# Kernel optimization log

Measured on AMD Instinct MI355X. Metric: run time of the kernel, lower is better.

Reference implementation:

```python
import jax, jax.numpy as jnp
import numpy as np

V, H, HALF, L, B = 32000, 512, 256, 1024, 64
LN_EPS = 1e-5
DELTA_EPS = 1e-6


def _forward(seq, embed, ff_w1, ff_b1, ff_w2, ff_b2, ln_g, ln_b,
             sem_w, sem_b, epi_w, epi_b, out_w, out_b):
    # Encoder: embed -> residual FFN -> LayerNorm
    e = embed[seq]                                   # (B, L, H)
    ff = jax.nn.relu(e @ ff_w1 + ff_b1) @ ff_w2 + ff_b2
    x = e + ff
    mu = jnp.mean(x, axis=-1, keepdims=True)
    var = jnp.mean((x - mu) ** 2, axis=-1, keepdims=True)
    h = (x - mu) / jnp.sqrt(var + LN_EPS) * ln_g + ln_b  # (B, L, H)

    # Project all timesteps at once (batched GEMM instead of per-step Linear)
    ks_all = h @ sem_w + sem_b                       # (B, L, half)
    ke_all = h @ epi_w + epi_b                       # (B, L, half)

    Bsz = seq.shape[0]
    Ls = seq.shape[1]
    w_t = jnp.arange(1, Ls, dtype=h.dtype) / Ls      # (L-1,) linear recency weights

    def step(carry, inp):
        M_s, M_e = carry
        k_s, k_e, w = inp                            # (B, half), (B, half), scalar
        vps = jnp.einsum('bij,bj->bi', M_s, k_s)
        dvs = k_s - vps / (jnp.sum(k_s * k_s, axis=-1, keepdims=True) + DELTA_EPS)
        M_s = M_s + dvs[:, :, None] * k_s[:, None, :]
        vpe = jnp.einsum('bij,bj->bi', M_e, k_e)
        dve = k_e - vpe / (jnp.sum(k_e * k_e, axis=-1, keepdims=True) + DELTA_EPS)
        M_e = M_e + w * (dve[:, :, None] * k_e[:, None, :])
        return (M_s, M_e), None

    M0 = jnp.zeros((Bsz, HALF, HALF), dtype=h.dtype)
    xs = (jnp.swapaxes(ks_all[:, :-1], 0, 1),        # (L-1, B, half)
          jnp.swapaxes(ke_all[:, :-1], 0, 1),
          w_t)
    (M_s, M_e), _ = jax.lax.scan(step, (M0, M0), xs)

    cs = jnp.einsum('bij,bj->bi', M_s, ks_all[:, -1])
    ce = jnp.einsum('bij,bj->bi', M_e, ke_all[:, -1])
    return jnp.concatenate([cs, ce], axis=-1) @ out_w + out_b  # (B, V)


def setup_inputs() -> dict:
    key = jax.random.key(0)
    ks = jax.random.split(key, 8)
    n = lambda k, shape, s=0.02: jax.random.normal(k, shape, jnp.float32) * s
    return {
        'seq': jax.random.randint(ks[0], (B, L), 0, V),
        'embed': n(ks[1], (V, H)),
        'ff_w1': n(ks[2], (H, 2 * H)), 'ff_b1': jnp.zeros((2 * H,), jnp.float32),
        'ff_w2': n(ks[3], (2 * H, H)), 'ff_b2': jnp.zeros((H,), jnp.float32),
        'ln_g': jnp.ones((H,), jnp.float32), 'ln_b': jnp.zeros((H,), jnp.float32),
        'sem_w': n(ks[4], (H, HALF)), 'sem_b': jnp.zeros((HALF,), jnp.float32),
        'epi_w': n(ks[5], (H, HALF)), 'epi_b': jnp.zeros((HALF,), jnp.float32),
        'out_w': n(ks[6], (2 * HALF, V)), 'out_b': jnp.zeros((V,), jnp.float32),
    }


def reference(seq, embed, ff_w1, ff_b1, ff_w2, ff_b2, ln_g, ln_b,
              sem_w, sem_b, epi_w, epi_b, out_w, out_b):
    return _forward(seq, embed, ff_w1, ff_b1, ff_w2, ff_b2, ln_g, ln_b,
                    sem_w, sem_b, epi_w, epi_b, out_w, out_b)
```

## Files before the change

### kernel.cpp

```cpp
#include <hip/hip_runtime.h>

typedef unsigned short ushort_t;
typedef unsigned int uint_t;
typedef __attribute__((ext_vector_type(8))) short short8;
typedef __attribute__((ext_vector_type(4))) float f32x4;

static constexpr int V = 32000, H = 512, HALFD = 256, LSEQ = 1024, BB = 64;

__device__ __forceinline__ ushort_t f2bf(float f) {
    uint_t u = __float_as_uint(f);
    u = (u + 0x7FFFu + ((u >> 16) & 1u)) >> 16;
    return (ushort_t)u;
}
__device__ __forceinline__ float bf2f(ushort_t u) {
    return __uint_as_float(((uint_t)u) << 16);
}
__device__ __forceinline__ float bflo(uint_t u) { return __uint_as_float(u << 16); }
__device__ __forceinline__ float bfhi(uint_t u) { return __uint_as_float(u & 0xffff0000u); }
__device__ __forceinline__ float bfres(float v) { return v - bf2f(f2bf(v)); }

typedef const __attribute__((address_space(1))) void* gas_ptr;
typedef __attribute__((address_space(3))) void* las_ptr;
#define GLDS16(g, l) __builtin_amdgcn_global_load_lds((gas_ptr)(g), (las_ptr)(l), 16, 0, 0)

__device__ __forceinline__ const short8* rd64(const ushort_t* b, int row, int chunk) {
    return (const short8*)(b + row * 32 + (((chunk ^ ((row >> 1) & 3)) & 3) << 3));
}
__device__ __forceinline__ ushort_t* wr64(ushort_t* b, int row, int chunk) {
    return b + row * 32 + (((chunk ^ ((row >> 1) & 3)) & 3) << 3);
}

__global__ void transpose_cvt(const float* __restrict__ W, ushort_t* __restrict__ Wt,
                              int K, int N) {
    __shared__ float tile[32][33];
    int k0 = blockIdx.y * 32, n0 = blockIdx.x * 32;
    int tx = threadIdx.x & 31, ty = threadIdx.x >> 5;
    #pragma unroll
    for (int i = 0; i < 32; i += 8)
        tile[ty + i][tx] = W[(size_t)(k0 + ty + i) * N + n0 + tx];
    __syncthreads();
    #pragma unroll
    for (int i = 0; i < 32; i += 8)
        Wt[(size_t)(n0 + ty + i) * K + k0 + tx] = f2bf(tile[tx][ty + i]);
}

__global__ __launch_bounds__(256) void gemm_ffn1(
        const int* __restrict__ seqp, const float* __restrict__ embed,
        const ushort_t* __restrict__ Bt, const float* __restrict__ bias,
        ushort_t* __restrict__ Cout, int N, int K) {
    __shared__ __align__(16) ushort_t Al[2048];
    __shared__ __align__(16) ushort_t Bl[4096];
    int t = threadIdx.x;
    int m0 = blockIdx.y * 64, n0 = blockIdx.x * 128;
    int lane = t & 63, wid = t >> 6;
    int wm = (wid & 1) * 32, wn = (wid >> 1) * 64;
    int lid = lane & 15, quad = lane >> 4;
    int srow = t >> 2;
    int gch = (t & 3) ^ ((t >> 3) & 3);

    int tok0 = seqp[m0 + srow];
    const float* e0 = embed + (size_t)tok0 * H + (t & 3) * 8;
    const ushort_t* b0p = Bt + (size_t)(n0 + srow) * K + gch * 8;
    const ushort_t* b1p = Bt + (size_t)(n0 + 64 + srow) * K + gch * 8;
    ushort_t* ldsB = Bl + wid * 512;
    ushort_t* aw0 = wr64(Al, srow, t & 3);

    f32x4 acc[2][4];
    #pragma unroll
    for (int i = 0; i < 2; ++i)
        #pragma unroll
        for (int j = 0; j < 4; ++j)
            acc[i][j] = (f32x4){0.f, 0.f, 0.f, 0.f};

    for (int k0 = 0; k0 < K; k0 += 32) {
        __syncthreads();
        GLDS16(b0p + k0, ldsB);
        GLDS16(b1p + k0, ldsB + 2048);
        float4 ea0 = *(const float4*)(e0 + k0);
        float4 eb0 = *(const float4*)(e0 + k0 + 4);
        short8 s0;
        s0[0] = (short)f2bf(ea0.x); s0[1] = (short)f2bf(ea0.y);
        s0[2] = (short)f2bf(ea0.z); s0[3] = (short)f2bf(ea0.w);
        s0[4] = (short)f2bf(eb0.x); s0[5] = (short)f2bf(eb0.y);
        s0[6] = (short)f2bf(eb0.z); s0[7] = (short)f2bf(eb0.w);
        *(short8*)aw0 = s0;
        __syncthreads();
        short8 af[2], bfr[4];
        #pragma unroll
        for (int i = 0; i < 2; ++i) af[i] = *rd64(Al, wm + i * 16 + lid, quad);
        #pragma unroll
        for (int i = 0; i < 4; ++i) bfr[i] = *rd64(Bl, wn + i * 16 + lid, quad);
        #pragma unroll
        for (int mt = 0; mt < 2; ++mt)
            #pragma unroll
            for (int nt = 0; nt < 4; ++nt)
                acc[mt][nt] = __builtin_amdgcn_mfma_f32_16x16x32_bf16(
                    af[mt], bfr[nt], acc[mt][nt], 0, 0, 0);
    }
    #pragma unroll
    for (int mt = 0; mt < 2; ++mt)
        #pragma unroll
        for (int nt = 0; nt < 4; ++nt)
            #pragma unroll
            for (int rg = 0; rg < 4; ++rg) {
                int row = m0 + wm + mt * 16 + quad * 4 + rg;
                int col = n0 + wn + nt * 16 + lid;
                float v = fmaxf(acc[mt][nt][rg] + bias[col], 0.f);
                Cout[(size_t)row * N + col] = f2bf(v);
            }
}

__global__ __launch_bounds__(256) void gemm_ffn2(
        const ushort_t* __restrict__ A, const ushort_t* __restrict__ Bt,
        const float* __restrict__ bias, const int* __restrict__ seqp,
        const float* __restrict__ embed, ushort_t* __restrict__ Cout,
        int N, int K) {
    __shared__ __align__(16) ushort_t Al[2048];
    __shared__ __align__(16) ushort_t Bl[4096];
    int t = threadIdx.x;
    int m0 = blockIdx.y * 64, n0 = blockIdx.x * 128;
    int lane = t & 63, wid = t >> 6;
    int wm = (wid & 1) * 32, wn = (wid >> 1) * 64;
    int lid = lane & 15, quad = lane >> 4;
    int srow = t >> 2;
    int gch = (t & 3) ^ ((t >> 3) & 3);

    const ushort_t* a0p = A + (size_t)(m0 + srow) * K + gch * 8;
    const ushort_t* b0p = Bt + (size_t)(n0 + srow) * K + gch * 8;
    const ushort_t* b1p = Bt + (size_t)(n0 + 64 + srow) * K + gch * 8;
    ushort_t* ldsA = Al + wid * 512;
    ushort_t* ldsB = Bl + wid * 512;

    f32x4 acc[2][4];
    #pragma unroll
    for (int i = 0; i < 2; ++i)
        #pragma unroll
        for (int j = 0; j < 4; ++j)
            acc[i][j] = (f32x4){0.f, 0.f, 0.f, 0.f};

    for (int k0 = 0; k0 < K; k0 += 32) {
        __syncthreads();
        GLDS16(a0p + k0, ldsA);
        GLDS16(b0p + k0, ldsB);
        GLDS16(b1p + k0, ldsB + 2048);
        __syncthreads();
        short8 af[2], bfr[4];
        #pragma unroll
        for (int i = 0; i < 2; ++i) af[i] = *rd64(Al, wm + i * 16 + lid, quad);
        #pragma unroll
        for (int i = 0; i < 4; ++i) bfr[i] = *rd64(Bl, wn + i * 16 + lid, quad);
        #pragma unroll
        for (int mt = 0; mt < 2; ++mt)
            #pragma unroll
            for (int nt = 0; nt < 4; ++nt)
                acc[mt][nt] = __builtin_amdgcn_mfma_f32_16x16x32_bf16(
                    af[mt], bfr[nt], acc[mt][nt], 0, 0, 0);
    }
    #pragma unroll
    for (int mt = 0; mt < 2; ++mt)
        #pragma unroll
        for (int rg = 0; rg < 4; ++rg) {
            int row = m0 + wm + mt * 16 + quad * 4 + rg;
            int tok = seqp[row];
            const float* erow = embed + (size_t)tok * H;
            #pragma unroll
            for (int nt = 0; nt < 4; ++nt) {
                int col = n0 + wn + nt * 16 + lid;
                float v = acc[mt][nt][rg] + bias[col] + erow[col];
                Cout[(size_t)row * N + col] = f2bf(v);
            }
        }
}

__global__ __launch_bounds__(256) void gemm_proj(
        const ushort_t* __restrict__ A, const ushort_t* __restrict__ Bt,
        const float* __restrict__ biasS, const float* __restrict__ biasE,
        ushort_t* __restrict__ outS, ushort_t* __restrict__ outE, int K) {
    __shared__ __align__(16) ushort_t Al[2048];
    __shared__ __align__(16) ushort_t Bl[4096];
    int t = threadIdx.x;
    int m0 = blockIdx.y * 64, n0 = blockIdx.x * 128;
    int lane = t & 63, wid = t >> 6;
    int wm = (wid & 1) * 32, wn = (wid >> 1) * 64;
    int lid = lane & 15, quad = lane >> 4;
    int srow = t >> 2;
    int gch = (t & 3) ^ ((t >> 3) & 3);

    const ushort_t* a0p = A + (size_t)(m0 + srow) * K + gch * 8;
    const ushort_t* b0p = Bt + (size_t)(n0 + srow) * K + gch * 8;
    const ushort_t* b1p = Bt + (size_t)(n0 + 64 + srow) * K + gch * 8;
    ushort_t* ldsA = Al + wid * 512;
    ushort_t* ldsB = Bl + wid * 512;

    f32x4 acc[2][4];
    #pragma unroll
    for (int i = 0; i < 2; ++i)
        #pragma unroll
        for (int j = 0; j < 4; ++j)
            acc[i][j] = (f32x4){0.f, 0.f, 0.f, 0.f};

    for (int k0 = 0; k0 < K; k0 += 32) {
        __syncthreads();
        GLDS16(a0p + k0, ldsA);
        GLDS16(b0p + k0, ldsB);
        GLDS16(b1p + k0, ldsB + 2048);
        __syncthreads();
        short8 af[2], bfr[4];
        #pragma unroll
        for (int i = 0; i < 2; ++i) af[i] = *rd64(Al, wm + i * 16 + lid, quad);
        #pragma unroll
        for (int i = 0; i < 4; ++i) bfr[i] = *rd64(Bl, wn + i * 16 + lid, quad);
        #pragma unroll
        for (int mt = 0; mt < 2; ++mt)
            #pragma unroll
            for (int nt = 0; nt < 4; ++nt)
                acc[mt][nt] = __builtin_amdgcn_mfma_f32_16x16x32_bf16(
                    af[mt], bfr[nt], acc[mt][nt], 0, 0, 0);
    }
    #pragma unroll
    for (int mt = 0; mt < 2; ++mt)
        #pragma unroll
        for (int nt = 0; nt < 4; ++nt)
            #pragma unroll
            for (int rg = 0; rg < 4; ++rg) {
                int row = m0 + wm + mt * 16 + quad * 4 + rg;
                int col = n0 + wn + nt * 16 + lid;
                if (col < 256)
                    outS[(size_t)row * HALFD + col] = f2bf(acc[mt][nt][rg] + biasS[col]);
                else
                    outE[(size_t)row * HALFD + col - 256] =
                        f2bf(acc[mt][nt][rg] + biasE[col - 256]);
            }
}

__global__ void ln_kernel(ushort_t* X, const float* __restrict__ g,
                          const float* __restrict__ bta) {
    int row = blockIdx.x * 4 + (threadIdx.x >> 6);
    int lane = threadIdx.x & 63;
    ushort_t* xr = X + (size_t)row * H + lane * 8;
    short8 xv = *(short8*)xr;
    float x[8];
    #pragma unroll
    for (int j = 0; j < 8; ++j) x[j] = bf2f((ushort_t)xv[j]);
    float s = 0.f, ss = 0.f;
    #pragma unroll
    for (int j = 0; j < 8; ++j) { s += x[j]; ss += x[j] * x[j]; }
    #pragma unroll
    for (int d = 1; d < 64; d <<= 1) { s += __shfl_xor(s, d); ss += __shfl_xor(ss, d); }
    float mu = s * (1.f / 512.f);
    float var = ss * (1.f / 512.f) - mu * mu;
    float rstd = rsqrtf(var + 1e-5f);
    float4 g0 = *(const float4*)(g + lane * 8);
    float4 g1 = *(const float4*)(g + lane * 8 + 4);
    float4 b0 = *(const float4*)(bta + lane * 8);
    float4 b1 = *(const float4*)(bta + lane * 8 + 4);
    float gg[8] = {g0.x, g0.y, g0.z, g0.w, g1.x, g1.y, g1.z, g1.w};
    float bb[8] = {b0.x, b0.y, b0.z, b0.w, b1.x, b1.y, b1.z, b1.w};
    short8 o;
    #pragma unroll
    for (int j = 0; j < 8; ++j)
        o[j] = (short)f2bf((x[j] - mu) * rstd * gg[j] + bb[j]);
    *(short8*)xr = o;
}

__global__ void beta_kernel(const ushort_t* __restrict__ k, float* __restrict__ beta) {
    int row = blockIdx.x * 4 + (threadIdx.x >> 6);
    int lane = threadIdx.x & 63;
    ushort4 a = *(const ushort4*)(k + (size_t)row * HALFD + lane * 4);
    float ax = bf2f(a.x), ay = bf2f(a.y), az = bf2f(a.z), aw = bf2f(a.w);
    float s = ax * ax + ay * ay + az * az + aw * aw;
    #pragma unroll
    for (int d = 1; d < 64; d <<= 1) s += __shfl_xor(s, d);
    if (lane == 0) beta[row] = s + 1e-6f;
}

__global__ __launch_bounds__(256) void tinv_kernel(
        const ushort_t* __restrict__ ks, const ushort_t* __restrict__ ke,
        const float* __restrict__ beta_s, const float* __restrict__ beta_e,
        ushort_t* __restrict__ Dg) {
    __shared__ __align__(16) ushort_t Kl[64][280];
    __shared__ __align__(16) ushort_t LmT[4][64][66];
    __shared__ float betsl[4][64];

    int t = threadIdx.x;
    int lane = t & 63, wv = t >> 6;
    int lid = lane & 15, quad = lane >> 4;
    int blk0 = blockIdx.x * 4;
    const float invL = 1.0f / 1024.0f;

    for (int pp = 0; pp < 4; ++pp) {
        int p = blk0 + pp;
        int ch = p & 15, bm = p >> 4;
        int mat = bm & 1, b = bm >> 1;
        const ushort_t* Kp = (mat ? ke : ks) + ((size_t)b * LSEQ + ch * 64) * HALFD;
        const float* Bp = (mat ? beta_e : beta_s) + (size_t)b * LSEQ + ch * 64;

        __syncthreads();
        {
            int j = t >> 2, c0 = (t & 3) * 64;
            const ushort_t* src = Kp + (size_t)j * HALFD + c0;
            #pragma unroll
            for (int x = 0; x < 8; ++x)
                *(short8*)&Kl[j][c0 + x * 8] = *(const short8*)(src + x * 8);
        }
        if (t < 64) betsl[pp][t] = Bp[t];
        __syncthreads();

        f32x4 g[4];
        #pragma unroll
        for (int i = 0; i < 4; ++i) g[i] = (f32x4){0.f, 0.f, 0.f, 0.f};
        #pragma unroll
        for (int kc = 0; kc < 8; ++kc) {
            short8 af = *(const short8*)&Kl[wv * 16 + lid][kc * 32 + quad * 8];
            #pragma unroll
            for (int nt = 0; nt < 4; ++nt) {
                short8 bq = *(const short8*)&Kl[nt * 16 + lid][kc * 32 + quad * 8];
                g[nt] = __builtin_amdgcn_mfma_f32_16x16x32_bf16(af, bq, g[nt], 0, 0, 0);
            }
        }
        #pragma unroll
        for (int nt = 0; nt < 4; ++nt)
            #pragma unroll
            for (int rg = 0; rg < 4; ++rg) {
                int i = wv * 16 + quad * 4 + rg;
                int j = nt * 16 + lid;
                int s = ch * 64 + i;
                float wgt = mat ? (float)(s + 1) * invL : 1.0f;
                if (s >= 1023) wgt = 0.f;
                float wb = wgt / betsl[pp][i];
                LmT[pp][j][i] = f2bf((j < i) ? g[nt][rg] * wb : 0.f);
            }
    }
    __syncthreads();

    const ushort_t (*Lp)[66] = LmT[wv];
    float a[64];
    #pragma unroll
    for (int x = 0; x < 32; ++x) {
        uint_t u = *(const uint_t*)&Lp[lane][x * 2];
        a[x * 2]     = -bflo(u);
        a[x * 2 + 1] = -bfhi(u);
    }
    #pragma unroll
    for (int j = 0; j < 63; ++j) {
        float dj = a[j];
        const ushort_t* rowj = Lp[j];
        #pragma unroll
        for (int ii = (j + 1) & ~1; ii < 64; ii += 2) {
            uint_t u = *(const uint_t*)&rowj[ii];
            if (ii > j) a[ii] -= bflo(u) * dj;
            a[ii + 1]        -= bfhi(u) * dj;
        }
    }
    size_t pbase = (size_t)(blk0 + wv) * 4096;
    #pragma unroll
    for (int i = 0; i < 64; ++i)
// ... 192 lines not shown
    }

    __syncthreads();
    float* vsc = (float*)RHSl;
    float kvv[4];
    #pragma unroll
    for (int nt = 0; nt < 4; ++nt)
        kvv[nt] = bf2f(Kl[63][wn + nt * 16 + lid]);
    #pragma unroll
    for (int mt = 0; mt < 4; ++mt)
        #pragma unroll
        for (int rg = 0; rg < 4; ++rg) {
            float p = acc[mt][0][rg] * kvv[0] + acc[mt][1][rg] * kvv[1]
                    + acc[mt][2][rg] * kvv[2] + acc[mt][3][rg] * kvv[3];
            p += __shfl_xor(p, 1); p += __shfl_xor(p, 2);
            p += __shfl_xor(p, 4); p += __shfl_xor(p, 8);
            if (lid == 0)
                vsc[(wid >> 1) * 128 + wm + mt * 16 + quad * 4 + rg] = p;
        }
    __syncthreads();
    if (t < 128) {
        float sum = vsc[t] + vsc[128 + t] + vsc[256 + t] + vsc[384 + t];
        c[(size_t)b * 512 + mat * 256 + half * 128 + t] = sum;
    }
}

__global__ __launch_bounds__(512) void out_gemm(
        const float* __restrict__ c, const float* __restrict__ W,
        const float* __restrict__ bias, float* __restrict__ out) {
    __shared__ __align__(16) float cl[16][512];
    int t = threadIdx.x;
    int lane = t & 63, w = t >> 6;
    int cb = blockIdx.x * 256;
    int rb = blockIdx.y * 16;

    #pragma unroll
    for (int i = 0; i < 4; ++i) {
        int idx = t + i * 512;
        int row = idx >> 7, c4 = (idx & 127) * 4;
        *(float4*)&cl[row][c4] = *(const float4*)(c + (size_t)(rb + row) * 512 + c4);
    }
    __syncthreads();

    const float* wp = W + cb + lane * 4;
    int r0 = w * 2;
    f32x4 a0 = (f32x4){0.f, 0.f, 0.f, 0.f};
    f32x4 a1 = (f32x4){0.f, 0.f, 0.f, 0.f};

    #pragma unroll 2
    for (int k = 0; k < 512; k += 4) {
        f32x4 w0 = *(const f32x4*)(wp + (size_t)(k + 0) * V);
        f32x4 w1 = *(const f32x4*)(wp + (size_t)(k + 1) * V);
        f32x4 w2 = *(const f32x4*)(wp + (size_t)(k + 2) * V);
        f32x4 w3 = *(const f32x4*)(wp + (size_t)(k + 3) * V);
        f32x4 ca = *(const f32x4*)&cl[r0][k];
        f32x4 cb4 = *(const f32x4*)&cl[r0 + 1][k];
        a0 += ca[0] * w0; a0 += ca[1] * w1; a0 += ca[2] * w2; a0 += ca[3] * w3;
        a1 += cb4[0] * w0; a1 += cb4[1] * w1; a1 += cb4[2] * w2; a1 += cb4[3] * w3;
    }
    f32x4 bv = *(const f32x4*)(bias + cb + lane * 4);
    *(f32x4*)(out + (size_t)(rb + r0) * V + cb + lane * 4) = a0 + bv;
    *(f32x4*)(out + (size_t)(rb + r0 + 1) * V + cb + lane * 4) = a1 + bv;
}

extern "C" void kernel_launch(void* const* d_in, const int* in_sizes, int n_in,
                              void* d_out, int out_size, void* d_ws, size_t ws_size,
                              hipStream_t stream) {
    const int*   seq    = (const int*)d_in[0];
    const float* embed  = (const float*)d_in[1];
    const float* ff_w1  = (const float*)d_in[2];
    const float* ff_b1  = (const float*)d_in[3];
    const float* ff_w2  = (const float*)d_in[4];
    const float* ff_b2  = (const float*)d_in[5];
    const float* ln_g   = (const float*)d_in[6];
    const float* ln_b   = (const float*)d_in[7];
    const float* sem_w  = (const float*)d_in[8];
    const float* sem_b  = (const float*)d_in[9];
    const float* epi_w  = (const float*)d_in[10];
    const float* epi_b  = (const float*)d_in[11];
    const float* out_w  = (const float*)d_in[12];
    const float* out_b  = (const float*)d_in[13];
    float* outp = (float*)d_out;

    const int ML = BB * LSEQ;
    int RCH;
    if      (ws_size >= 271712256ull) RCH = 65536;
    else if (ws_size >= 120717312ull) RCH = 16384;
    else                              RCH = 8192;

    char* w = (char*)d_ws;
    size_t off = 0;
    ushort_t* ks_bf = (ushort_t*)(w + off); off += 33554432;
    ushort_t* ke_bf = (ushort_t*)(w + off); off += 33554432;
    ushort_t* ebc   = (ushort_t*)(w + off); off += (size_t)RCH * 512 * 2;
    ushort_t* t1c   = (ushort_t*)(w + off); off += (size_t)RCH * 1024 * 2;
    ushort_t* w1t   = (ushort_t*)(w + off); off += 1048576;
    ushort_t* w2t   = (ushort_t*)(w + off); off += 1048576;
    ushort_t* semt  = (ushort_t*)(w + off); off += 262144;
    ushort_t* epit  = (ushort_t*)(w + off); off += 262144;
    float*    bet_s = (float*)(w + off);    off += 262144;
    float*    bet_e = (float*)(w + off);    off += 262144;
    float*    cbuf  = (float*)(w + off);    off += 131072;
    ushort_t* Dbuf  = ebc;
    (void)t1c;

    transpose_cvt<<<dim3(1024 / 32, 512 / 32), 256, 0, stream>>>(ff_w1, w1t, 512, 1024);
    transpose_cvt<<<dim3(512 / 32, 1024 / 32), 256, 0, stream>>>(ff_w2, w2t, 1024, 512);
    transpose_cvt<<<dim3(256 / 32, 512 / 32), 256, 0, stream>>>(sem_w, semt, 512, 256);
    transpose_cvt<<<dim3(256 / 32, 512 / 32), 256, 0, stream>>>(epi_w, epit, 512, 256);

    for (int cc = 0; cc < ML / RCH; ++cc) {
        int c0 = cc * RCH;
        gemm_ffn1<<<dim3(1024 / 128, RCH / 64), 256, 0, stream>>>(
            seq + c0, embed, w1t, ff_b1, t1c, 1024, 512);
        gemm_ffn2<<<dim3(512 / 128, RCH / 64), 256, 0, stream>>>(
            t1c, w2t, ff_b2, seq + c0, embed, ebc, 512, 1024);
        ln_kernel<<<RCH / 4, 256, 0, stream>>>(ebc, ln_g, ln_b);
        gemm_proj<<<dim3(512 / 128, RCH / 64), 256, 0, stream>>>(
            ebc, semt, sem_b, epi_b,
            ks_bf + (size_t)c0 * HALFD, ke_bf + (size_t)c0 * HALFD, 512);
    }

    beta_kernel<<<ML / 4, 256, 0, stream>>>(ks_bf, bet_s);
    beta_kernel<<<ML / 4, 256, 0, stream>>>(ke_bf, bet_e);

    tinv_kernel<<<512, 256, 0, stream>>>(ks_bf, ke_bf, bet_s, bet_e, Dbuf);
    scan_kernel<<<256, 512, 0, stream>>>(ks_bf, ke_bf, bet_s, bet_e, Dbuf, cbuf);

    out_gemm<<<dim3(125, 4), 512, 0, stream>>>(cbuf, out_w, out_b, outp);
}
```

Before: 927.5 us.

## Double-buffer GEMM LDS tiles with 64-wide K steps in encoder GEMMs

The three encoder GEMM kernels (FFN1, FFN2, projection) now use two LDS buffers and a K step of 64 instead of 32. The next tile's global-to-LDS loads are issued before the MFMAs on the current tile, and there is one barrier per iteration instead of two. The XOR swizzle is widened to 8 chunks to match the 64-element rows. This is meant to hide global load latency and cut synchronisation overhead, at the cost of four times more LDS per block, which may reduce occupancy.

```diff
diff --git a/kernel.cpp b/kernel.cpp
--- a/kernel.cpp
+++ b/kernel.cpp
@@ -23,12 +23,6 @@
 typedef __attribute__((address_space(3))) void* las_ptr;
 #define GLDS16(g, l) __builtin_amdgcn_global_load_lds((gas_ptr)(g), (las_ptr)(l), 16, 0, 0)
 
-__device__ __forceinline__ const short8* rd64(const ushort_t* b, int row, int chunk) {
-    return (const short8*)(b + row * 32 + (((chunk ^ ((row >> 1) & 3)) & 3) << 3));
-}
-__device__ __forceinline__ ushort_t* wr64(ushort_t* b, int row, int chunk) {
-    return b + row * 32 + (((chunk ^ ((row >> 1) & 3)) & 3) << 3);
-}
 
 __global__ void transpose_cvt(const float* __restrict__ W, ushort_t* __restrict__ Wt,
                               int K, int N) {
@@ -48,22 +42,21 @@
         const int* __restrict__ seqp, const float* __restrict__ embed,
         const ushort_t* __restrict__ Bt, const float* __restrict__ bias,
         ushort_t* __restrict__ Cout, int N, int K) {
-    __shared__ __align__(16) ushort_t Al[2048];
-    __shared__ __align__(16) ushort_t Bl[4096];
+    __shared__ __align__(16) ushort_t Al[2][4096];
+    __shared__ __align__(16) ushort_t Bl[2][8192];
     int t = threadIdx.x;
     int m0 = blockIdx.y * 64, n0 = blockIdx.x * 128;
     int lane = t & 63, wid = t >> 6;
     int wm = (wid & 1) * 32, wn = (wid >> 1) * 64;
     int lid = lane & 15, quad = lane >> 4;
-    int srow = t >> 2;
-    int gch = (t & 3) ^ ((t >> 3) & 3);
-
-    int tok0 = seqp[m0 + srow];
-    const float* e0 = embed + (size_t)tok0 * H + (t & 3) * 8;
-    const ushort_t* b0p = Bt + (size_t)(n0 + srow) * K + gch * 8;
-    const ushort_t* b1p = Bt + (size_t)(n0 + 64 + srow) * K + gch * 8;
-    ushort_t* ldsB = Bl + wid * 512;
-    ushort_t* aw0 = wr64(Al, srow, t & 3);
+
+    int gch = (t & 7) ^ ((t >> 3) & 7);
+    const ushort_t* bp = Bt + (size_t)(n0 + (t >> 3)) * K + gch * 8;
+    int arow = t >> 2;
+    int tok = seqp[m0 + arow];
+    const float* ep = embed + (size_t)tok * H + (t & 3) * 16;
+    int aoff0 = arow * 64 + ((((t & 3) * 2) ^ (arow & 7)) << 3);
+    int aoff1 = arow * 64 + (((((t & 3) * 2) | 1) ^ (arow & 7)) << 3);
 
     f32x4 acc[2][4];
     #pragma unroll
@@ -72,31 +65,55 @@
         for (int j = 0; j < 4; ++j)
             acc[i][j] = (f32x4){0.f, 0.f, 0.f, 0.f};
 
-    for (int k0 = 0; k0 < K; k0 += 32) {
-        __syncthreads();
-        GLDS16(b0p + k0, ldsB);
-        GLDS16(b1p + k0, ldsB + 2048);
-        float4 ea0 = *(const float4*)(e0 + k0);
-        float4 eb0 = *(const float4*)(e0 + k0 + 4);
-        short8 s0;
-        s0[0] = (short)f2bf(ea0.x); s0[1] = (short)f2bf(ea0.y);
-        s0[2] = (short)f2bf(ea0.z); s0[3] = (short)f2bf(ea0.w);
-        s0[4] = (short)f2bf(eb0.x); s0[5] = (short)f2bf(eb0.y);
-        s0[6] = (short)f2bf(eb0.z); s0[7] = (short)f2bf(eb0.w);
-        *(short8*)aw0 = s0;
-        __syncthreads();
-        short8 af[2], bfr[4];
-        #pragma unroll
-        for (int i = 0; i < 2; ++i) af[i] = *rd64(Al, wm + i * 16 + lid, quad);
-        #pragma unroll
-        for (int i = 0; i < 4; ++i) bfr[i] = *rd64(Bl, wn + i * 16 + lid, quad);
-        #pragma unroll
-        for (int mt = 0; mt < 2; ++mt)
-            #pragma unroll
-            for (int nt = 0; nt < 4; ++nt)
-                acc[mt][nt] = __builtin_amdgcn_mfma_f32_16x16x32_bf16(
-                    af[mt], bfr[nt], acc[mt][nt], 0, 0, 0);
-    }
+#define FFN1_STAGE(bufi, k)                                                   \
+    {                                                                         \
+        GLDS16(bp + (k),           &Bl[bufi][wid * 512]);                     \
+        GLDS16(bp + (k) + 32 * K,  &Bl[bufi][wid * 512 + 2048]);              \
+        GLDS16(bp + (k) + 64 * K,  &Bl[bufi][wid * 512 + 4096]);              \
+        GLDS16(bp + (k) + 96 * K,  &Bl[bufi][wid * 512 + 6144]);              \
+        float4 f0 = *(const float4*)(ep + (k));                               \
+        float4 f1 = *(const float4*)(ep + (k) + 4);                           \
+        float4 f2 = *(const float4*)(ep + (k) + 8);                           \
+        float4 f3 = *(const float4*)(ep + (k) + 12);                          \
+        short8 s0, s1;                                                        \
+        s0[0] = (short)f2bf(f0.x); s0[1] = (short)f2bf(f0.y);                 \
+        s0[2] = (short)f2bf(f0.z); s0[3] = (short)f2bf(f0.w);                 \
+        s0[4] = (short)f2bf(f1.x); s0[5] = (short)f2bf(f1.y);                 \
+        s0[6] = (short)f2bf(f1.z); s0[7] = (short)f2bf(f1.w);                 \
+        s1[0] = (short)f2bf(f2.x); s1[1] = (short)f2bf(f2.y);                 \
+        s1[2] = (short)f2bf(f2.z); s1[3] = (short)f2bf(f2.w);                 \
+        s1[4] = (short)f2bf(f3.x); s1[5] = (short)f2bf(f3.y);                 \
+        s1[6] = (short)f2bf(f3.z); s1[7] = (short)f2bf(f3.w);                 \
+        *(short8*)&Al[bufi][aoff0] = s0;                                      \
+        *(short8*)&Al[bufi][aoff1] = s1;                                      \
+    }
+
+    int nk = K / 64;
+    FFN1_STAGE(0, 0);
+    __syncthreads();
+    for (int ks = 0; ks < nk; ++ks) {
+        int cur = ks & 1;
+        if (ks + 1 < nk) FFN1_STAGE(cur ^ 1, (ks + 1) * 64);
+        #pragma unroll
+        for (int kc = 0; kc < 2; ++kc) {
+            int sl = (((kc << 2) | quad) ^ (lid & 7)) << 3;
+            short8 af[2], bfr[4];
+            #pragma unroll
+            for (int i = 0; i < 2; ++i)
+                af[i] = *(const short8*)&Al[cur][(wm + i * 16 + lid) * 64 + sl];
+            #pragma unroll
+            for (int i = 0; i < 4; ++i)
+                bfr[i] = *(const short8*)&Bl[cur][(wn + i * 16 + lid) * 64 + sl];
+            #pragma unroll
+            for (int mt = 0; mt < 2; ++mt)
+                #pragma unroll
+                for (int nt = 0; nt < 4; ++nt)
+                    acc[mt][nt] = __builtin_amdgcn_mfma_f32_16x16x32_bf16(
+                        af[mt], bfr[nt], acc[mt][nt], 0, 0, 0);
+        }
+        __syncthreads();
+    }
+#undef FFN1_STAGE
     #pragma unroll
     for (int mt = 0; mt < 2; ++mt)
         #pragma unroll
@@ -115,21 +132,17 @@
         const float* __restrict__ bias, const int* __restrict__ seqp,
         const float* __restrict__ embed, ushort_t* __restrict__ Cout,
         int N, int K) {
-    __shared__ __align__(16) ushort_t Al[2048];
-    __shared__ __align__(16) ushort_t Bl[4096];
+    __shared__ __align__(16) ushort_t Al[2][4096];
+    __shared__ __align__(16) ushort_t Bl[2][8192];
     int t = threadIdx.x;
     int m0 = blockIdx.y * 64, n0 = blockIdx.x * 128;
     int lane = t & 63, wid = t >> 6;
     int wm = (wid & 1) * 32, wn = (wid >> 1) * 64;
     int lid = lane & 15, quad = lane >> 4;
-    int srow = t >> 2;
-    int gch = (t & 3) ^ ((t >> 3) & 3);
-
-    const ushort_t* a0p = A + (size_t)(m0 + srow) * K + gch * 8;
-    const ushort_t* b0p = Bt + (size_t)(n0 + srow) * K + gch * 8;
-    const ushort_t* b1p = Bt + (size_t)(n0 + 64 + srow) * K + gch * 8;
-    ushort_t* ldsA = Al + wid * 512;
-    ushort_t* ldsB = Bl + wid * 512;
+
+    int gch = (t & 7) ^ ((t >> 3) & 7);
+    const ushort_t* ap = A + (size_t)(m0 + (t >> 3)) * K + gch * 8;
+    const ushort_t* bp = Bt + (size_t)(n0 + (t >> 3)) * K + gch * 8;
 
     f32x4 acc[2][4];
     #pragma unroll
@@ -138,24 +151,42 @@
         for (int j = 0; j < 4; ++j)
             acc[i][j] = (f32x4){0.f, 0.f, 0.f, 0.f};
 
-    for (int k0 = 0; k0 < K; k0 += 32) {
-        __syncthreads();
-        GLDS16(a0p + k0, ldsA);
-        GLDS16(b0p + k0, ldsB);
-        GLDS16(b1p + k0, ldsB + 2048);
-        __syncthreads();
-        short8 af[2], bfr[4];
-        #pragma unroll
-        for (int i = 0; i < 2; ++i) af[i] = *rd64(Al, wm + i * 16 + lid, quad);
-        #pragma unroll
-        for (int i = 0; i < 4; ++i) bfr[i] = *rd64(Bl, wn + i * 16 + lid, quad);
-        #pragma unroll
-        for (int mt = 0; mt < 2; ++mt)
-            #pragma unroll
-            for (int nt = 0; nt < 4; ++nt)
-                acc[mt][nt] = __builtin_amdgcn_mfma_f32_16x16x32_bf16(
-                    af[mt], bfr[nt], acc[mt][nt], 0, 0, 0);
-    }
+#define G2_STAGE(bufi, k)                                                     \
+    {                                                                         \
+        GLDS16(ap + (k),           &Al[bufi][wid * 512]);                     \
+        GLDS16(ap + (k) + 32 * K,  &Al[bufi][wid * 512 + 2048]);              \
+        GLDS16(bp + (k),           &Bl[bufi][wid * 512]);                     \
+        GLDS16(bp + (k) + 32 * K,  &Bl[bufi][wid * 512 + 2048]);              \
+        GLDS16(bp + (k) + 64 * K,  &Bl[bufi][wid * 512 + 4096]);              \
+        GLDS16(bp + (k) + 96 * K,  &Bl[bufi][wid * 512 + 6144]);              \
+    }
+
+    int nk = K / 64;
+    G2_STAGE(0, 0);
+    __syncthreads();
+    for (int ks = 0; ks < nk; ++ks) {
+        int cur = ks & 1;
+        if (ks + 1 < nk) G2_STAGE(cur ^ 1, (ks + 1) * 64);
+        #pragma unroll
+        for (int kc = 0; kc < 2; ++kc) {
+            int sl = (((kc << 2) | quad) ^ (lid & 7)) << 3;
+            short8 af[2], bfr[4];
+            #pragma unroll
+            for (int i = 0; i < 2; ++i)
+                af[i] = *(const short8*)&Al[cur][(wm + i * 16 + lid) * 64 + sl];
+            #pragma unroll
+            for (int i = 0; i < 4; ++i)
+                bfr[i] = *(const short8*)&Bl[cur][(wn + i * 16 + lid) * 64 + sl];
+            #pragma unroll
+            for (int mt = 0; mt < 2; ++mt)
+                #pragma unroll
+                for (int nt = 0; nt < 4; ++nt)
+                    acc[mt][nt] = __builtin_amdgcn_mfma_f32_16x16x32_bf16(
+                        af[mt], bfr[nt], acc[mt][nt], 0, 0, 0);
+        }
+        __syncthreads();
+    }
+#undef G2_STAGE
     #pragma unroll
     for (int mt = 0; mt < 2; ++mt)
         #pragma unroll
@@ -176,21 +207,17 @@
         const ushort_t* __restrict__ A, const ushort_t* __restrict__ Bt,
         const float* __restrict__ biasS, const float* __restrict__ biasE,
         ushort_t* __restrict__ outS, ushort_t* __restrict__ outE, int K) {
-    __shared__ __align__(16) ushort_t Al[2048];
-    __shared__ __align__(16) ushort_t Bl[4096];
+    __shared__ __align__(16) ushort_t Al[2][4096];
+    __shared__ __align__(16) ushort_t Bl[2][8192];
     int t = threadIdx.x;
     int m0 = blockIdx.y * 64, n0 = blockIdx.x * 128;
     int lane = t & 63, wid = t >> 6;
     int wm = (wid & 1) * 32, wn = (wid >> 1) * 64;
     int lid = lane & 15, quad = lane >> 4;
-    int srow = t >> 2;
-    int gch = (t & 3) ^ ((t >> 3) & 3);
-
-    const ushort_t* a0p = A + (size_t)(m0 + srow) * K + gch * 8;
-    const ushort_t* b0p = Bt + (size_t)(n0 + srow) * K + gch * 8;
-    const ushort_t* b1p = Bt + (size_t)(n0 + 64 + srow) * K + gch * 8;
-    ushort_t* ldsA = Al + wid * 512;
-    ushort_t* ldsB = Bl + wid * 512;
+
+    int gch = (t & 7) ^ ((t >> 3) & 7);
+    const ushort_t* ap = A + (size_t)(m0 + (t >> 3)) * K + gch * 8;
+    const ushort_t* bp = Bt + (size_t)(n0 + (t >> 3)) * K + gch * 8;
 
     f32x4 acc[2][4];
     #pragma unroll
@@ -199,24 +226,42 @@
         for (int j = 0; j < 4; ++j)
             acc[i][j] = (f32x4){0.f, 0.f, 0.f, 0.f};
 
-    for (int k0 = 0; k0 < K; k0 += 32) {
-        __syncthreads();
-        GLDS16(a0p + k0, ldsA);
-        GLDS16(b0p + k0, ldsB);
-        GLDS16(b1p + k0, ldsB + 2048);
-        __syncthreads();
-        short8 af[2], bfr[4];
-        #pragma unroll
-        for (int i = 0; i < 2; ++i) af[i] = *rd64(Al, wm + i * 16 + lid, quad);
-        #pragma unroll
-        for (int i = 0; i < 4; ++i) bfr[i] = *rd64(Bl, wn + i * 16 + lid, quad);
-        #pragma unroll
-        for (int mt = 0; mt < 2; ++mt)
-            #pragma unroll
-            for (int nt = 0; nt < 4; ++nt)
-                acc[mt][nt] = __builtin_amdgcn_mfma_f32_16x16x32_bf16(
-                    af[mt], bfr[nt], acc[mt][nt], 0, 0, 0);
-    }
+#define GP_STAGE(bufi, k)                                                     \
+    {                                                                         \
+        GLDS16(ap + (k),           &Al[bufi][wid * 512]);                     \
+        GLDS16(ap + (k) + 32 * K,  &Al[bufi][wid * 512 + 2048]);              \
+        GLDS16(bp + (k),           &Bl[bufi][wid * 512]);                     \
+        GLDS16(bp + (k) + 32 * K,  &Bl[bufi][wid * 512 + 2048]);              \
+        GLDS16(bp + (k) + 64 * K,  &Bl[bufi][wid * 512 + 4096]);              \
+        GLDS16(bp + (k) + 96 * K,  &Bl[bufi][wid * 512 + 6144]);              \
+    }
+
+    int nk = K / 64;
+    GP_STAGE(0, 0);
+    __syncthreads();
+    for (int ks = 0; ks < nk; ++ks) {
+        int cur = ks & 1;
+        if (ks + 1 < nk) GP_STAGE(cur ^ 1, (ks + 1) * 64);
+        #pragma unroll
+        for (int kc = 0; kc < 2; ++kc) {
+            int sl = (((kc << 2) | quad) ^ (lid & 7)) << 3;
+            short8 af[2], bfr[4];
+            #pragma unroll
+            for (int i = 0; i < 2; ++i)
+                af[i] = *(const short8*)&Al[cur][(wm + i * 16 + lid) * 64 + sl];
+            #pragma unroll
+            for (int i = 0; i < 4; ++i)
+                bfr[i] = *(const short8*)&Bl[cur][(wn + i * 16 + lid) * 64 + sl];
+            #pragma unroll
+            for (int mt = 0; mt < 2; ++mt)
+                #pragma unroll
+                for (int nt = 0; nt < 4; ++nt)
+                    acc[mt][nt] = __builtin_amdgcn_mfma_f32_16x16x32_bf16(
+                        af[mt], bfr[nt], acc[mt][nt], 0, 0, 0);
+        }
+        __syncthreads();
+    }
+#undef GP_STAGE
     #pragma unroll
     for (int mt = 0; mt < 2; ++mt)
         #pragma unroll
```

After: 922.0 us. About the same (-0.6%).

## Fuse encoder FFN, LayerNorm, projections and key norms into one kernel

Applied to the files above, without the earlier changes.

Replaces the chunked sequence of FFN1, FFN2, LayerNorm, projection GEMM and beta-norm kernels with a single kernel per 64-row tile. The embedding rows, the FFN hidden activations and the normalized output stay in LDS, and the key squared norms are computed in the epilogue. This removes global round-trips of the 1024-wide hidden activations and the LN output, plus several launches. In exchange each block re-streams all weight matrices through LDS with plain loads and no double buffering, uses large LDS (lower occupancy), and launches only 1024 blocks. Dbuf now gets its own workspace region, so the workspace must be large enough to hold it.

```diff
diff --git a/kernel.cpp b/kernel.cpp
--- a/kernel.cpp
+++ b/kernel.cpp
@@ -17,18 +17,6 @@
 }
 __device__ __forceinline__ float bflo(uint_t u) { return __uint_as_float(u << 16); }
 __device__ __forceinline__ float bfhi(uint_t u) { return __uint_as_float(u & 0xffff0000u); }
-__device__ __forceinline__ float bfres(float v) { return v - bf2f(f2bf(v)); }
-
-typedef const __attribute__((address_space(1))) void* gas_ptr;
-typedef __attribute__((address_space(3))) void* las_ptr;
-#define GLDS16(g, l) __builtin_amdgcn_global_load_lds((gas_ptr)(g), (las_ptr)(l), 16, 0, 0)
-
-__device__ __forceinline__ const short8* rd64(const ushort_t* b, int row, int chunk) {
-    return (const short8*)(b + row * 32 + (((chunk ^ ((row >> 1) & 3)) & 3) << 3));
-}
-__device__ __forceinline__ ushort_t* wr64(ushort_t* b, int row, int chunk) {
-    return b + row * 32 + (((chunk ^ ((row >> 1) & 3)) & 3) << 3);
-}
 
 __global__ void transpose_cvt(const float* __restrict__ W, ushort_t* __restrict__ Wt,
                               int K, int N) {
@@ -44,234 +32,236 @@
         Wt[(size_t)(n0 + ty + i) * K + k0 + tx] = f2bf(tile[tx][ty + i]);
 }
 
-__global__ __launch_bounds__(256) void gemm_ffn1(
+__global__ __launch_bounds__(512) void enc_fused(
         const int* __restrict__ seqp, const float* __restrict__ embed,
-        const ushort_t* __restrict__ Bt, const float* __restrict__ bias,
-        ushort_t* __restrict__ Cout, int N, int K) {
-    __shared__ __align__(16) ushort_t Al[2048];
-    __shared__ __align__(16) ushort_t Bl[4096];
+        const ushort_t* __restrict__ W1t, const ushort_t* __restrict__ W2t,
+        const float* __restrict__ b1, const float* __restrict__ b2,
+        const float* __restrict__ lng, const float* __restrict__ lnb,
+        const ushort_t* __restrict__ Pt,
+        const float* __restrict__ biasS, const float* __restrict__ biasE,
+        ushort_t* __restrict__ outS, ushort_t* __restrict__ outE,
+        float* __restrict__ bet_s, float* __restrict__ bet_e) {
+    __shared__ __align__(16) ushort_t El[64 * 520];
+    __shared__ __align__(16) ushort_t T1l[64 * 264];
+    __shared__ __align__(16) ushort_t Bst[512 * 40];
+    __shared__ int toks[64];
+    __shared__ float lnP[64 * 8], lnQ[64 * 8];
+    __shared__ float lnM[64], lnR[64];
+
     int t = threadIdx.x;
-    int m0 = blockIdx.y * 64, n0 = blockIdx.x * 128;
-    int lane = t & 63, wid = t >> 6;
-    int wm = (wid & 1) * 32, wn = (wid >> 1) * 64;
+    int lane = t & 63, w = t >> 6;
     int lid = lane & 15, quad = lane >> 4;
-    int srow = t >> 2;
-    int gch = (t & 3) ^ ((t >> 3) & 3);
-
-    int tok0 = seqp[m0 + srow];
-    const float* e0 = embed + (size_t)tok0 * H + (t & 3) * 8;
-    const ushort_t* b0p = Bt + (size_t)(n0 + srow) * K + gch * 8;
-    const ushort_t* b1p = Bt + (size_t)(n0 + 64 + srow) * K + gch * 8;
-    ushort_t* ldsB = Bl + wid * 512;
-    ushort_t* aw0 = wr64(Al, srow, t & 3);
-
-    f32x4 acc[2][4];
-    #pragma unroll
-    for (int i = 0; i < 2; ++i)
+    int m0 = blockIdx.x * 64;
+
+    if (t < 64) toks[t] = seqp[m0 + t];
+    {
+        int r = t >> 3, c0 = (t & 7) * 64;
+        const float* e = embed + (size_t)seqp[m0 + r] * H + c0;
+        #pragma unroll
+        for (int j = 0; j < 8; ++j) {
+            float4 a = *(const float4*)(e + j * 8);
+            float4 bq = *(const float4*)(e + j * 8 + 4);
+            short8 sv;
+            sv[0] = (short)f2bf(a.x);  sv[1] = (short)f2bf(a.y);
+            sv[2] = (short)f2bf(a.z);  sv[3] = (short)f2bf(a.w);
+            sv[4] = (short)f2bf(bq.x); sv[5] = (short)f2bf(bq.y);
+            sv[6] = (short)f2bf(bq.z); sv[7] = (short)f2bf(bq.w);
+            *(short8*)&El[r * 520 + c0 + j * 8] = sv;
+        }
+    }
+
+    f32x4 acc2[4][4];
+    #pragma unroll
+    for (int i = 0; i < 4; ++i)
         #pragma unroll
         for (int j = 0; j < 4; ++j)
-            acc[i][j] = (f32x4){0.f, 0.f, 0.f, 0.f};
-
-    for (int k0 = 0; k0 < K; k0 += 32) {
-        __syncthreads();
-        GLDS16(b0p + k0, ldsB);
-        GLDS16(b1p + k0, ldsB + 2048);
-        float4 ea0 = *(const float4*)(e0 + k0);
-        float4 eb0 = *(const float4*)(e0 + k0 + 4);
-        short8 s0;
-        s0[0] = (short)f2bf(ea0.x); s0[1] = (short)f2bf(ea0.y);
-        s0[2] = (short)f2bf(ea0.z); s0[3] = (short)f2bf(ea0.w);
-        s0[4] = (short)f2bf(eb0.x); s0[5] = (short)f2bf(eb0.y);
-        s0[6] = (short)f2bf(eb0.z); s0[7] = (short)f2bf(eb0.w);
-        *(short8*)aw0 = s0;
-        __syncthreads();
-        short8 af[2], bfr[4];
-        #pragma unroll
-        for (int i = 0; i < 2; ++i) af[i] = *rd64(Al, wm + i * 16 + lid, quad);
-        #pragma unroll
-        for (int i = 0; i < 4; ++i) bfr[i] = *rd64(Bl, wn + i * 16 + lid, quad);
-        #pragma unroll
-        for (int mt = 0; mt < 2; ++mt)
+            acc2[i][j] = (f32x4){0.f, 0.f, 0.f, 0.f};
+    __syncthreads();
+
+    for (int s = 0; s < 4; ++s) {
+        f32x4 acc1[4][2];
+        #pragma unroll
+        for (int i = 0; i < 4; ++i)
+            #pragma unroll
+            for (int j = 0; j < 2; ++j)
+                acc1[i][j] = (f32x4){0.f, 0.f, 0.f, 0.f};
+        for (int kc = 0; kc < 16; ++kc) {
+            {
+                int r = t >> 1, ko = (t & 1) * 16;
+                const ushort_t* src = W1t + (size_t)(s * 256 + r) * 512 + kc * 32 + ko;
+                *(short8*)&Bst[r * 40 + ko]     = *(const short8*)(src);
+                *(short8*)&Bst[r * 40 + ko + 8] = *(const short8*)(src + 8);
+            }
+            __syncthreads();
+            short8 af[4], bfr[2];
+            #pragma unroll
+            for (int i = 0; i < 4; ++i)
+                af[i] = *(const short8*)&El[(i * 16 + lid) * 520 + kc * 32 + quad * 8];
+            #pragma unroll
+            for (int i = 0; i < 2; ++i)
+                bfr[i] = *(const short8*)&Bst[(w * 32 + i * 16 + lid) * 40 + quad * 8];
+            #pragma unroll
+            for (int mt = 0; mt < 4; ++mt)
+                #pragma unroll
+                for (int nt = 0; nt < 2; ++nt)
+                    acc1[mt][nt] = __builtin_amdgcn_mfma_f32_16x16x32_bf16(
+                        af[mt], bfr[nt], acc1[mt][nt], 0, 0, 0);
+            __syncthreads();
+        }
+        #pragma unroll
+        for (int mt = 0; mt < 4; ++mt)
+            #pragma unroll
+            for (int nt = 0; nt < 2; ++nt) {
+                int col = w * 32 + nt * 16 + lid;
+                float bc = b1[s * 256 + col];
+                #pragma unroll
+                for (int rg = 0; rg < 4; ++rg) {
+                    int row = mt * 16 + quad * 4 + rg;
+                    T1l[row * 264 + col] = f2bf(fmaxf(acc1[mt][nt][rg] + bc, 0.f));
+                }
+            }
+        for (int kc = 0; kc < 8; ++kc) {
+            {
+                const ushort_t* src = W2t + (size_t)t * 1024 + s * 256 + kc * 32;
+                #pragma unroll
+                for (int j = 0; j < 4; ++j)
+                    *(short8*)&Bst[t * 40 + j * 8] = *(const short8*)(src + j * 8);
+            }
+            __syncthreads();
+            short8 af[4], bfr[4];
+            #pragma unroll
+            for (int i = 0; i < 4; ++i)
+                af[i] = *(const short8*)&T1l[(i * 16 + lid) * 264 + kc * 32 + quad * 8];
+            #pragma unroll
+            for (int i = 0; i < 4; ++i)
+                bfr[i] = *(const short8*)&Bst[(w * 64 + i * 16 + lid) * 40 + quad * 8];
+            #pragma unroll
+            for (int mt = 0; mt < 4; ++mt)
+                #pragma unroll
+                for (int nt = 0; nt < 4; ++nt)
+                    acc2[mt][nt] = __builtin_amdgcn_mfma_f32_16x16x32_bf16(
+                        af[mt], bfr[nt], acc2[mt][nt], 0, 0, 0);
+            __syncthreads();
+        }
+    }
+
+    #pragma unroll
+    for (int mt = 0; mt < 4; ++mt)
+        #pragma unroll
+        for (int rg = 0; rg < 4; ++rg) {
+            int row = mt * 16 + quad * 4 + rg;
+            const float* er = embed + (size_t)toks[row] * H;
+            #pragma unroll
+            for (int nt = 0; nt < 4; ++nt) {
+                int col = w * 64 + nt * 16 + lid;
+                acc2[mt][nt][rg] += b2[col] + er[col];
+            }
+        }
+    #pragma unroll
+    for (int mt = 0; mt < 4; ++mt)
+        #pragma unroll
+        for (int rg = 0; rg < 4; ++rg) {
+            float sv = 0.f, qv = 0.f;
+            #pragma unroll
+            for (int nt = 0; nt < 4; ++nt) {
+                float v = acc2[mt][nt][rg];
+                sv += v; qv += v * v;
+            }
+            #pragma unroll
+            for (int d = 1; d < 16; d <<= 1) {
+                sv += __shfl_xor(sv, d);
+                qv += __shfl_xor(qv, d);
+            }
+            int row = mt * 16 + quad * 4 + rg;
+            if (lid == 0) { lnP[row * 8 + w] = sv; lnQ[row * 8 + w] = qv; }
+        }
+    __syncthreads();
+    if (t < 64) {
+        float sv = 0.f, qv = 0.f;
+        #pragma unroll
+        for (int j = 0; j < 8; ++j) { sv += lnP[t * 8 + j]; qv += lnQ[t * 8 + j]; }
+        float mu = sv * (1.f / 512.f);
+        float var = qv * (1.f / 512.f) - mu * mu;
+        lnM[t] = mu;
+        lnR[t] = rsqrtf(var + 1e-5f);
+    }
+    __syncthreads();
+    #pragma unroll
+    for (int mt = 0; mt < 4; ++mt)
+        #pragma unroll
+        for (int rg = 0; rg < 4; ++rg) {
+            int row = mt * 16 + quad * 4 + rg;
+            float mu = lnM[row], rs = lnR[row];
+            #pragma unroll
+            for (int nt = 0; nt < 4; ++nt) {
+                int col = w * 64 + nt * 16 + lid;
+                El[row * 520 + col] =
+                    f2bf((acc2[mt][nt][rg] - mu) * rs * lng[col] + lnb[col]);
+            }
+        }
+    __syncthreads();
+
+    f32x4 acc3[4][4];
+    #pragma unroll
+    for (int i = 0; i < 4; ++i)
+        #pragma unroll
+        for (int j = 0; j < 4; ++j)
+            acc3[i][j] = (f32x4){0.f, 0.f, 0.f, 0.f};
+    for (int kc = 0; kc < 16; ++kc) {
+        {
+            const ushort_t* src = Pt + (size_t)t * 512 + kc * 32;
+            #pragma unroll
+            for (int j = 0; j < 4; ++j)
+                *(short8*)&Bst[t * 40 + j * 8] = *(const short8*)(src + j * 8);
+        }
+        __syncthreads();
+        short8 af[4], bfr[4];
+        #pragma unroll
+        for (int i = 0; i < 4; ++i)
+            af[i] = *(const short8*)&El[(i * 16 + lid) * 520 + kc * 32 + quad * 8];
+        #pragma unroll
+        for (int i = 0; i < 4; ++i)
+            bfr[i] = *(const short8*)&Bst[(w * 64 + i * 16 + lid) * 40 + quad * 8];
+        #pragma unroll
+        for (int mt = 0; mt < 4; ++mt)
             #pragma unroll
             for (int nt = 0; nt < 4; ++nt)
-                acc[mt][nt] = __builtin_amdgcn_mfma_f32_16x16x32_bf16(
-                    af[mt], bfr[nt], acc[mt][nt], 0, 0, 0);
-    }
-    #pragma unroll
-    for (int mt = 0; mt < 2; ++mt)
-        #pragma unroll
-        for (int nt = 0; nt < 4; ++nt)
+                acc3[mt][nt] = __builtin_amdgcn_mfma_f32_16x16x32_bf16(
+                    af[mt], bfr[nt], acc3[mt][nt], 0, 0, 0);
+        __syncthreads();
+    }
+    {
+        const float* bb = (w < 4) ? (biasS + w * 64) : (biasE + (w - 4) * 64);
+        ushort_t* op = (w < 4) ? outS : outE;
+        int cbase = (w < 4) ? (w * 64) : ((w - 4) * 64);
+        #pragma unroll
+        for (int mt = 0; mt < 4; ++mt)
             #pragma unroll
             for (int rg = 0; rg < 4; ++rg) {
-                int row = m0 + wm + mt * 16 + quad * 4 + rg;
-                int col = n0 + wn + nt * 16 + lid;
-                float v = fmaxf(acc[mt][nt][rg] + bias[col], 0.f);
-                Cout[(size_t)row * N + col] = f2bf(v);
-            }
-}
-
-__global__ __launch_bounds__(256) void gemm_ffn2(
-        const ushort_t* __restrict__ A, const ushort_t* __restrict__ Bt,
-        const float* __restrict__ bias, const int* __restrict__ seqp,
-        const float* __restrict__ embed, ushort_t* __restrict__ Cout,
-        int N, int K) {
-    __shared__ __align__(16) ushort_t Al[2048];
-    __shared__ __align__(16) ushort_t Bl[4096];
-    int t = threadIdx.x;
-    int m0 = blockIdx.y * 64, n0 = blockIdx.x * 128;
-    int lane = t & 63, wid = t >> 6;
-    int wm = (wid & 1) * 32, wn = (wid >> 1) * 64;
-    int lid = lane & 15, quad = lane >> 4;
-    int srow = t >> 2;
-    int gch = (t & 3) ^ ((t >> 3) & 3);
-
-    const ushort_t* a0p = A + (size_t)(m0 + srow) * K + gch * 8;
-    const ushort_t* b0p = Bt + (size_t)(n0 + srow) * K + gch * 8;
-    const ushort_t* b1p = Bt + (size_t)(n0 + 64 + srow) * K + gch * 8;
-    ushort_t* ldsA = Al + wid * 512;
-    ushort_t* ldsB = Bl + wid * 512;
-
-    f32x4 acc[2][4];
-    #pragma unroll
-    for (int i = 0; i < 2; ++i)
-        #pragma unroll
-        for (int j = 0; j < 4; ++j)
-            acc[i][j] = (f32x4){0.f, 0.f, 0.f, 0.f};
-
-    for (int k0 = 0; k0 < K; k0 += 32) {
-        __syncthreads();
-        GLDS16(a0p + k0, ldsA);
-        GLDS16(b0p + k0, ldsB);
-        GLDS16(b1p + k0, ldsB + 2048);
-        __syncthreads();
-        short8 af[2], bfr[4];
-        #pragma unroll
-        for (int i = 0; i < 2; ++i) af[i] = *rd64(Al, wm + i * 16 + lid, quad);
-        #pragma unroll
-        for (int i = 0; i < 4; ++i) bfr[i] = *rd64(Bl, wn + i * 16 + lid, quad);
-        #pragma unroll
-        for (int mt = 0; mt < 2; ++mt)
-            #pragma unroll
-            for (int nt = 0; nt < 4; ++nt)
-                acc[mt][nt] = __builtin_amdgcn_mfma_f32_16x16x32_bf16(
-                    af[mt], bfr[nt], acc[mt][nt], 0, 0, 0);
-    }
-    #pragma unroll
-    for (int mt = 0; mt < 2; ++mt)
-        #pragma unroll
-        for (int rg = 0; rg < 4; ++rg) {
-            int row = m0 + wm + mt * 16 + quad * 4 + rg;
-            int tok = seqp[row];
-            const float* erow = embed + (size_t)tok * H;
-            #pragma unroll
-            for (int nt = 0; nt < 4; ++nt) {
-                int col = n0 + wn + nt * 16 + lid;
-                float v = acc[mt][nt][rg] + bias[col] + erow[col];
-                Cout[(size_t)row * N + col] = f2bf(v);
-            }
-        }
-}
-
-__global__ __launch_bounds__(256) void gemm_proj(
-        const ushort_t* __restrict__ A, const ushort_t* __restrict__ Bt,
-        const float* __restrict__ biasS, const float* __restrict__ biasE,
-        ushort_t* __restrict__ outS, ushort_t* __restrict__ outE, int K) {
-    __shared__ __align__(16) ushort_t Al[2048];
-    __shared__ __align__(16) ushort_t Bl[4096];
-    int t = threadIdx.x;
-    int m0 = blockIdx.y * 64, n0 = blockIdx.x * 128;
-    int lane = t & 63, wid = t >> 6;
-    int wm = (wid & 1) * 32, wn = (wid >> 1) * 64;
-    int lid = lane & 15, quad = lane >> 4;
-    int srow = t >> 2;
-    int gch = (t & 3) ^ ((t >> 3) & 3);
-
-    const ushort_t* a0p = A + (size_t)(m0 + srow) * K + gch * 8;
-    const ushort_t* b0p = Bt + (size_t)(n0 + srow) * K + gch * 8;
-    const ushort_t* b1p = Bt + (size_t)(n0 + 64 + srow) * K + gch * 8;
-    ushort_t* ldsA = Al + wid * 512;
-    ushort_t* ldsB = Bl + wid * 512;
-
-    f32x4 acc[2][4];
-    #pragma unroll
-    for (int i = 0; i < 2; ++i)
-        #pragma unroll
-        for (int j = 0; j < 4; ++j)
-            acc[i][j] = (f32x4){0.f, 0.f, 0.f, 0.f};
-
-    for (int k0 = 0; k0 < K; k0 += 32) {
-        __syncthreads();
-        GLDS16(a0p + k0, ldsA);
-        GLDS16(b0p + k0, ldsB);
-        GLDS16(b1p + k0, ldsB + 2048);
-        __syncthreads();
-        short8 af[2], bfr[4];
-        #pragma unroll
-        for (int i = 0; i < 2; ++i) af[i] = *rd64(Al, wm + i * 16 + lid, quad);
-        #pragma unroll
-        for (int i = 0; i < 4; ++i) bfr[i] = *rd64(Bl, wn + i * 16 + lid, quad);
-        #pragma unroll
-        for (int mt = 0; mt < 2; ++mt)
-            #pragma unroll
-            for (int nt = 0; nt < 4; ++nt)
-                acc[mt][nt] = __builtin_amdgcn_mfma_f32_16x16x32_bf16(
-                    af[mt], bfr[nt], acc[mt][nt], 0, 0, 0);
-    }
-    #pragma unroll
-    for (int mt = 0; mt < 2; ++mt)
-        #pragma unroll
-        for (int nt = 0; nt < 4; ++nt)
-            #pragma unroll
-            for (int rg = 0; rg < 4; ++rg) {
-                int row = m0 + wm + mt * 16 + quad * 4 + rg;
-                int col = n0 + wn + nt * 16 + lid;
-                if (col < 256)
-                    outS[(size_t)row * HALFD + col] = f2bf(acc[mt][nt][rg] + biasS[col]);
-                else
-                    outE[(size_t)row * HALFD + col - 256] =
-                        f2bf(acc[mt][nt][rg] + biasE[col - 256]);
-            }
-}
-
-__global__ void ln_kernel(ushort_t* X, const float* __restrict__ g,
-                          const float* __restrict__ bta) {
-    int row = blockIdx.x * 4 + (threadIdx.x >> 6);
-    int lane = threadIdx.x & 63;
-    ushort_t* xr = X + (size_t)row * H + lane * 8;
-    short8 xv = *(short8*)xr;
-    float x[8];
-    #pragma unroll
-    for (int j = 0; j < 8; ++j) x[j] = bf2f((ushort_t)xv[j]);
-    float s = 0.f, ss = 0.f;
-    #pragma unroll
-    for (int j = 0; j < 8; ++j) { s += x[j]; ss += x[j] * x[j]; }
-    #pragma unroll
-    for (int d = 1; d < 64; d <<= 1) { s += __shfl_xor(s, d); ss += __shfl_xor(ss, d); }
-    float mu = s * (1.f / 512.f);
-    float var = ss * (1.f / 512.f) - mu * mu;
-    float rstd = rsqrtf(var + 1e-5f);
-    float4 g0 = *(const float4*)(g + lane * 8);
-    float4 g1 = *(const float4*)(g + lane * 8 + 4);
-    float4 b0 = *(const float4*)(bta + lane * 8);
-    float4 b1 = *(const float4*)(bta + lane * 8 + 4);
-    float gg[8] = {g0.x, g0.y, g0.z, g0.w, g1.x, g1.y, g1.z, g1.w};
-    float bb[8] = {b0.x, b0.y, b0.z, b0.w, b1.x, b1.y, b1.z, b1.w};
-    short8 o;
-    #pragma unroll
-    for (int j = 0; j < 8; ++j)
-        o[j] = (short)f2bf((x[j] - mu) * rstd * gg[j] + bb[j]);
-    *(short8*)xr = o;
-}
-
-__global__ void beta_kernel(const ushort_t* __restrict__ k, float* __restrict__ beta) {
-    int row = blockIdx.x * 4 + (threadIdx.x >> 6);
-    int lane = threadIdx.x & 63;
-    ushort4 a = *(const ushort4*)(k + (size_t)row * HALFD + lane * 4);
-    float ax = bf2f(a.x), ay = bf2f(a.y), az = bf2f(a.z), aw = bf2f(a.w);
-    float s = ax * ax + ay * ay + az * az + aw * aw;
-    #pragma unroll
-    for (int d = 1; d < 64; d <<= 1) s += __shfl_xor(s, d);
-    if (lane == 0) beta[row] = s + 1e-6f;
+                int row = mt * 16 + quad * 4 + rg;
+                float sq = 0.f;
+                #pragma unroll
+                for (int nt = 0; nt < 4; ++nt) {
+                    int c = nt * 16 + lid;
+                    ushort_t hv = f2bf(acc3[mt][nt][rg] + bb[c]);
+                    op[(size_t)(m0 + row) * HALFD + cbase + c] = hv;
+                    float fv = bf2f(hv);
+                    sq += fv * fv;
+                }
+                #pragma unroll
+                for (int d = 1; d < 16; d <<= 1) sq += __shfl_xor(sq, d);
+                if (lid == 0) lnP[row * 8 + w] = sq;
+            }
+        __syncthreads();
+        if (t < 128) {
+            int row = t & 63;
+            int w0 = (t < 64) ? 0 : 4;
+            float sv = lnP[row * 8 + w0] + lnP[row * 8 + w0 + 1]
+                     + lnP[row * 8 + w0 + 2] + lnP[row * 8 + w0 + 3];
+            float* bout = (t < 64) ? bet_s : bet_e;
+            bout[m0 + row] = sv + 1e-6f;
+        }
+    }
 }
 
 __global__ __launch_bounds__(256) void tinv_kernel(
@@ -630,18 +620,10 @@
     const float* out_b  = (const float*)d_in[13];
     float* outp = (float*)d_out;
 
-    const int ML = BB * LSEQ;
-    int RCH;
-    if      (ws_size >= 271712256ull) RCH = 65536;
-    else if (ws_size >= 120717312ull) RCH = 16384;
-    else                              RCH = 8192;
-
     char* w = (char*)d_ws;
     size_t off = 0;
     ushort_t* ks_bf = (ushort_t*)(w + off); off += 33554432;
     ushort_t* ke_bf = (ushort_t*)(w + off); off += 33554432;
-    ushort_t* ebc   = (ushort_t*)(w + off); off += (size_t)RCH * 512 * 2;
-    ushort_t* t1c   = (ushort_t*)(w + off); off += (size_t)RCH * 1024 * 2;
     ushort_t* w1t   = (ushort_t*)(w + off); off += 1048576;
     ushort_t* w2t   = (ushort_t*)(w + off); off += 1048576;
     ushort_t* semt  = (ushort_t*)(w + off); off += 262144;
@@ -649,28 +631,16 @@
     float*    bet_s = (float*)(w + off);    off += 262144;
     float*    bet_e = (float*)(w + off);    off += 262144;
     float*    cbuf  = (float*)(w + off);    off += 131072;
-    ushort_t* Dbuf  = ebc;
-    (void)t1c;
+    ushort_t* Dbuf  = (ushort_t*)(w + off); off += 16777216;
 
     transpose_cvt<<<dim3(1024 / 32, 512 / 32), 256, 0, stream>>>(ff_w1, w1t, 512, 1024);
     transpose_cvt<<<dim3(512 / 32, 1024 / 32), 256, 0, stream>>>(ff_w2, w2t, 1024, 512);
     transpose_cvt<<<dim3(256 / 32, 512 / 32), 256, 0, stream>>>(sem_w, semt, 512, 256);
     transpose_cvt<<<dim3(256 / 32, 512 / 32), 256, 0, stream>>>(epi_w, epit, 512, 256);
 
-    for (int cc = 0; cc < ML / RCH; ++cc) {
-        int c0 = cc * RCH;
-        gemm_ffn1<<<dim3(1024 / 128, RCH / 64), 256, 0, stream>>>(
-            seq + c0, embed, w1t, ff_b1, t1c, 1024, 512);
-        gemm_ffn2<<<dim3(512 / 128, RCH / 64), 256, 0, stream>>>(
-            t1c, w2t, ff_b2, seq + c0, embed, ebc, 512, 1024);
-        ln_kernel<<<RCH / 4, 256, 0, stream>>>(ebc, ln_g, ln_b);
-        gemm_proj<<<dim3(512 / 128, RCH / 64), 256, 0, stream>>>(
-            ebc, semt, sem_b, epi_b,
-            ks_bf + (size_t)c0 * HALFD, ke_bf + (size_t)c0 * HALFD, 512);
-    }
-
-    beta_kernel<<<ML / 4, 256, 0, stream>>>(ks_bf, bet_s);
-    beta_kernel<<<ML / 4, 256, 0, stream>>>(ke_bf, bet_e);
+    enc_fused<<<1024, 512, 0, stream>>>(
+        seq, embed, w1t, w2t, ff_b1, ff_b2, ln_g, ln_b,
+        semt, sem_b, epi_b, ks_bf, ke_bf, bet_s, bet_e);
 
     tinv_kernel<<<512, 256, 0, stream>>>(ks_bf, ke_bf, bet_s, bet_e, Dbuf);
     scan_kernel<<<256, 512, 0, stream>>>(ks_bf, ke_bf, bet_s, bet_e, Dbuf, cbuf);
```

After: 962.6 us. 3.8% more time.
